# Kernel tuning notes

Hardware: AMD Instinct MI355X
Metric: run time of the kernel (lower is better)

The kernel has to match this reference:

```python
import jax, jax.numpy as jnp
import numpy as np
from functools import partial

M_HEADS, N_LEVELS, N_POINTS = 4, 3, 4


def conv2d(x, w, b, padding=1, dilation=1):
    y = jax.lax.conv_general_dilated(
        x, w, window_strides=(1, 1),
        padding=[(padding, padding), (padding, padding)],
        rhs_dilation=(dilation, dilation),
        dimension_numbers=('NCHW', 'OIHW', 'NCHW'))
    return y + b[None, :, None, None]


def lrelu(x):
    return jnp.where(x >= 0, x, 0.1 * x)


def _bilinear(img, gx, gy, zero_pad):
    # img: (C,H,W); gx,gy: arbitrary shape of pixel coordinates
    C, H, W = img.shape
    x0 = jnp.floor(gx); y0 = jnp.floor(gy)
    wx = gx - x0; wy = gy - y0
    def g(xi, yi):
        xc = jnp.clip(xi, 0, W - 1).astype(jnp.int32)
        yc = jnp.clip(yi, 0, H - 1).astype(jnp.int32)
        v = img[:, yc, xc]  # (C, ...)
        if zero_pad:
            ok = ((xi >= 0) & (xi <= W - 1) & (yi >= 0) & (yi <= H - 1)).astype(img.dtype)
            v = v * ok
        return v
    return (g(x0, y0) * ((1 - wx) * (1 - wy)) + g(x0 + 1, y0) * (wx * (1 - wy))
            + g(x0, y0 + 1) * ((1 - wx) * wy) + g(x0 + 1, y0 + 1) * (wx * wy))


def warp(x, flo):
    # torch grid_sample(padding_mode='border', align_corners=True) at coords grid+flow
    B, C, H, W = x.shape
    yy, xx = jnp.meshgrid(jnp.arange(H, dtype=x.dtype), jnp.arange(W, dtype=x.dtype), indexing='ij')
    gx = xx[None] + flo[:, 0]
    gy = yy[None] + flo[:, 1]
    return jax.vmap(partial(_bilinear, zero_pad=False))(x, gx, gy)


def _forward(frame, srcframe, flow_forward, flow_backward,
             emb_qk_w, emb_qk_b, emb_v_w, emb_v_b, so_w, so_b, aw_w, aw_b,
             vp_w, vp_b, op_w, op_b, ff_w, ff_b, ffn1_w, ffn1_b, ffn2_w, ffn2_b,
             fus_w, fus_b):
    M, L, P = M_HEADS, N_LEVELS, N_POINTS
    b, t, c, h, w = frame.shape
    HW = h * w
    D = c // M
    # flow-warped neighbor frames -> query embedding
    warp01 = warp(frame[:, 0], flow_backward[:, 0])
    warp21 = warp(frame[:, 2], flow_forward[:, 1])
    q_in = jnp.concatenate([warp01, frame[:, 1], warp21, flow_forward[:, 1], flow_backward[:, 0]], axis=1)
    query = lrelu(conv2d(q_in, emb_qk_w, emb_qk_b))  # (b, 3c, h, w)
    value = lrelu(conv2d(frame.reshape(b, t * c, h, w), emb_v_w, emb_v_b)).reshape(b, t, c, h, w)
    # MSDeformAttn_Fusion
    v = conv2d(value.reshape(b * t, c, h, w), vp_w, vp_b).reshape(b, t, c, h, w)  # value_proj per frame
    off = conv2d(query, so_w, so_b)   # (b, M*L*P*2, h, w)
    aw = conv2d(query, aw_w, aw_b)    # (b, M*L*P,   h, w)
    off = off.reshape(b, M * L * P * 2, HW).transpose(0, 2, 1).reshape(b, HW, M, L, P, 2)
    attn = aw.reshape(b, M * L * P, HW).transpose(0, 2, 1).reshape(b, HW, M, L * P)
    attn = jax.nn.softmax(attn, axis=-1).reshape(b, HW, M, L, P)
    # flow-guided offsets: [flow_backward10, 0, flow_forward12] per level
    flow_stack = jnp.stack([flow_backward[:, 0], jnp.zeros_like(flow_forward[:, 1]), flow_forward[:, 1]], axis=2)  # (b,2,L,h,w)
    off = off + flow_stack.reshape(b, 2, L, HW).transpose(0, 3, 2, 1)[:, :, None, :, None, :]
    # normalized reference points (valid ratios are all ones)
    ys, xs = jnp.meshgrid(jnp.arange(h, dtype=frame.dtype) + 0.5,
                          jnp.arange(w, dtype=frame.dtype) + 0.5, indexing='ij')
    ref = jnp.stack([xs.reshape(-1) / w, ys.reshape(-1) / h], axis=-1)  # (HW, 2)
    norm = jnp.array([w, h], dtype=frame.dtype)
    loc = ref[None, :, None, None, None, :] + off / norm  # (b,HW,M,L,P,2) in [0,1]
    # deformable gather: grid_sample(mode=bilinear, padding=zeros, align_corners=False)
    imgs = v.reshape(b, L, M, D, h, w).transpose(0, 2, 1, 3, 4, 5).reshape(b * M * L, D, h, w)
    locs = loc.transpose(0, 2, 3, 1, 4, 5).reshape(b * M * L, HW, P, 2)
    gx = locs[..., 0] * w - 0.5   # align_corners=False pixel coords
    gy = locs[..., 1] * h - 0.5
    sampled = jax.vmap(partial(_bilinear, zero_pad=True))(imgs, gx, gy)  # (b*M*L, D, HW, P)
    sampled = sampled.reshape(b, M, L, D, HW, P)
    out = jnp.einsum('nmldqp,nqmlp->nqmd', sampled, attn).reshape(b, HW, c)
    out = out.reshape(b, h, w, c).transpose(0, 3, 1, 2)
    out = conv2d(out, op_w, op_b)  # output_proj
    # post-attention feed-forward + fusion
    out = conv2d(out, ff_w, ff_b) + frame[:, 1]
    ffn = lrelu(conv2d(jnp.concatenate([out, srcframe[:, 1]], axis=1), ffn1_w, ffn1_b, padding=2, dilation=2))
    out = out + conv2d(ffn, ffn2_w, ffn2_b)
    out = lrelu(conv2d(out, fus_w, fus_b, padding=0))
    return out


def setup_inputs() -> dict:
    key = jax.random.key(0)
    ks = jax.random.split(key, 28)
    b, t, c, h, w = 2, 3, 32, 256, 256
    M, L, P = M_HEADS, N_LEVELS, N_POINTS
    def rn(k, shape, s=1.0):
        return jax.random.normal(k, shape, dtype=jnp.float32) * s
    return {
        'frame': rn(ks[0], (b, t, c, h, w)),
        'srcframe': rn(ks[1], (b, t, c, h, w)),
        'flow_forward': rn(ks[2], (b, 2, 2, h, w), 2.0),
        'flow_backward': rn(ks[3], (b, 2, 2, h, w), 2.0),
        'emb_qk_w': rn(ks[4], (3 * c, 3 * c + 4, 3, 3), 0.05), 'emb_qk_b': rn(ks[5], (3 * c,), 0.02),
        'emb_v_w': rn(ks[6], (3 * c, 3 * c, 3, 3), 0.05), 'emb_v_b': rn(ks[7], (3 * c,), 0.02),
        'so_w': rn(ks[8], (M * L * P * 2, 3 * c, 3, 3), 0.01), 'so_b': rn(ks[9], (M * L * P * 2,), 0.5),
        'aw_w': rn(ks[10], (M * L * P, 3 * c, 3, 3), 0.05), 'aw_b': rn(ks[11], (M * L * P,), 0.02),
        'vp_w': rn(ks[12], (c, c, 3, 3), 0.05), 'vp_b': rn(ks[13], (c,), 0.02),
        'op_w': rn(ks[14], (c, c, 3, 3), 0.05), 'op_b': rn(ks[15], (c,), 0.02),
        'ff_w': rn(ks[16], (c, c, 3, 3), 0.05), 'ff_b': rn(ks[17], (c,), 0.02),
        'ffn1_w': rn(ks[18], (c, 2 * c, 3, 3), 0.05), 'ffn1_b': rn(ks[19], (c,), 0.02),
        'ffn2_w': rn(ks[20], (c, c, 3, 3), 0.05), 'ffn2_b': rn(ks[21], (c,), 0.02),
        'fus_w': rn(ks[22], (c, c, 1, 1), 0.05), 'fus_b': rn(ks[23], (c,), 0.02),
    }


def reference(frame, srcframe, flow_forward, flow_backward,
              emb_qk_w, emb_qk_b, emb_v_w, emb_v_b, so_w, so_b, aw_w, aw_b,
              vp_w, vp_b, op_w, op_b, ff_w, ff_b, ffn1_w, ffn1_b, ffn2_w, ffn2_b,
              fus_w, fus_b):
    return _forward(frame, srcframe, flow_forward, flow_backward,
                    emb_qk_w, emb_qk_b, emb_v_w, emb_v_b, so_w, so_b, aw_w, aw_b,
                    vp_w, vp_b, op_w, op_b, ff_w, ff_b, ffn1_w, ffn1_b, ffn2_w, ffn2_b,
                    fus_w, fus_b)
```

## Files before the change

### kernel.cpp

```cpp
#include <hip/hip_runtime.h>
#include <cmath>

typedef _Float16 half_t;
typedef _Float16 half8 __attribute__((ext_vector_type(8)));
typedef _Float16 half4 __attribute__((ext_vector_type(4)));
typedef float floatx4 __attribute__((ext_vector_type(4)));

__device__ __forceinline__ float lrelu_f(float v) { return v >= 0.f ? v : 0.1f * v; }

template <int CIN, int COTOT>
__device__ __forceinline__ void pack_one(const float* __restrict__ w,
                                         half_t* __restrict__ o,
                                         int co_off, int co_n, int i)
{
    constexpr int NCB = (CIN + 31) / 32;
    int ci = i & 31;
    int t = i >> 5;
    int col = t % co_n; t /= co_n;
    int cb = t % NCB;
    int tap = t / NCB;
    int cg = cb * 32 + ci;
    float v = (cg < CIN) ? w[((long)col * CIN + cg) * 9 + tap] : 0.f;
    o[(((long)tap * NCB + cb) * COTOT + co_off + col) * 32 + ci] = (half_t)v;
}

__global__ __launch_bounds__(256) void prep_w_all(
    const float* __restrict__ qk, const float* __restrict__ ev,
    const float* __restrict__ so, const float* __restrict__ aw,
    const float* __restrict__ vp, const float* __restrict__ op,
    const float* __restrict__ ffw, const float* __restrict__ f1,
    const float* __restrict__ f2,
    half_t* wq, half_t* wv, half_t* wsoaw, half_t* wvp2, half_t* wop2,
    half_t* wff2, half_t* wffn1, half_t* wffn2)
{
    int i = blockIdx.x * 256 + threadIdx.x;
    constexpr int C0 = 110592;
    constexpr int C1 = C0 + 82944;
    constexpr int C2 = C1 + 82944;
    constexpr int C3 = C2 + 41472;
    constexpr int C4 = C3 + 9216;
    constexpr int C5 = C4 + 9216;
    constexpr int C6 = C5 + 9216;
    constexpr int C7 = C6 + 18432;
    constexpr int C8 = C7 + 9216;
    if (i < C0)      pack_one<100, 96>(qk, wq, 0, 96, i);
    else if (i < C1) pack_one<96, 96>(ev, wv, 0, 96, i - C0);
    else if (i < C2) pack_one<96, 144>(so, wsoaw, 0, 96, i - C1);
    else if (i < C3) pack_one<96, 144>(aw, wsoaw, 96, 48, i - C2);
    else if (i < C4) pack_one<32, 32>(vp, wvp2, 0, 32, i - C3);
    else if (i < C5) pack_one<32, 32>(op, wop2, 0, 32, i - C4);
    else if (i < C6) pack_one<32, 32>(ffw, wff2, 0, 32, i - C5);
    else if (i < C7) pack_one<64, 32>(f1, wffn1, 0, 32, i - C6);
    else if (i < C8) pack_one<32, 32>(f2, wffn2, 0, 32, i - C7);
}

__global__ __launch_bounds__(256) void copy_cl_kernel(
    const float* __restrict__ frame, const float* __restrict__ srcframe,
    const float* __restrict__ ff, const float* __restrict__ fb,
    half_t* __restrict__ qin, half_t* __restrict__ fcl,
    half_t* __restrict__ o3rec, int H, int W)
{
    const int HW = H * W;
    const int p = threadIdx.x >> 2, sub = threadIdx.x & 3;
    const int q = blockIdx.x * 64 + p;
    const int b = blockIdx.y;
    const long fbase = (long)b * 96 * HW;
    const long rq = ((long)b * HW + q) * 112;
    const long rf = ((long)b * HW + q) * 96;
    const long r3 = ((long)b * HW + q) * 64;

    half8 c0, c2;
    #pragma unroll
    for (int d = 0; d < 8; ++d) {
        c0[d] = (half_t)frame[fbase + (long)(sub * 8 + d) * HW + q];
        c2[d] = (half_t)frame[fbase + (long)(64 + sub * 8 + d) * HW + q];
    }
    *(half8*)&fcl[rf + sub * 8] = c0;
    *(half8*)&fcl[rf + 64 + sub * 8] = c2;

    half8 fv, sv;
    #pragma unroll
    for (int d = 0; d < 8; ++d) {
        long off = fbase + (long)(32 + sub * 8 + d) * HW + q;
        fv[d] = (half_t)frame[off];
        sv[d] = (half_t)srcframe[off];
    }
    *(half8*)&qin[rq + 32 + sub * 8] = fv;
    *(half8*)&fcl[rf + 32 + sub * 8] = fv;
    *(half8*)&o3rec[r3 + 32 + sub * 8] = sv;

    if (sub == 0) {
        half8 fl = {};
        fl[0] = (half_t)ff[((long)(b * 2 + 1) * 2 + 0) * HW + q];
        fl[1] = (half_t)ff[((long)(b * 2 + 1) * 2 + 1) * HW + q];
        fl[2] = (half_t)fb[((long)(b * 2 + 0) * 2 + 0) * HW + q];
        fl[3] = (half_t)fb[((long)(b * 2 + 0) * 2 + 1) * HW + q];
        *(half8*)&qin[rq + 96] = fl;
    } else if (sub == 1) {
        half8 z = {};
        *(half8*)&qin[rq + 104] = z;
    }
}

__global__ __launch_bounds__(256) void warp_cl_kernel(
    const half_t* __restrict__ fcl, const float* __restrict__ ff,
    const float* __restrict__ fb, half_t* __restrict__ qin, int H, int W)
{
    const int HW = H * W;
    const int p = threadIdx.x >> 2, sub = threadIdx.x & 3;
    const int q = blockIdx.x * 64 + p;
    const int b = blockIdx.y;
    const int x = q % W, y = q / W;
    const long rq = ((long)b * HW + q) * 112;
    const half_t* fc = fcl + (long)b * HW * 96;

    const float fb0x = fb[((long)(b * 2 + 0) * 2 + 0) * HW + q];
    const float fb0y = fb[((long)(b * 2 + 0) * 2 + 1) * HW + q];
    const float ff1x = ff[((long)(b * 2 + 1) * 2 + 0) * HW + q];
    const float ff1y = ff[((long)(b * 2 + 1) * 2 + 1) * HW + q];

    #pragma unroll
    for (int t = 0; t < 2; ++t) {
        const float fx = t ? ff1x : fb0x;
        const float fy = t ? ff1y : fb0y;
        const int coff = t ? 64 : 0;
        float gx = (float)x + fx, gy = (float)y + fy;
        float x0f = floorf(gx), y0f = floorf(gy);
        float wx = gx - x0f, wy = gy - y0f;
        int x0 = min(max((int)x0f, 0), W - 1);
        int x1 = min(max((int)x0f + 1, 0), W - 1);
        int y0 = min(max((int)y0f, 0), H - 1);
        int y1 = min(max((int)y0f + 1, 0), H - 1);
        float w00 = (1.f - wx) * (1.f - wy), w10 = wx * (1.f - wy);
        float w01 = (1.f - wx) * wy, w11 = wx * wy;

        half8 v00 = *(const half8*)&fc[(long)(y0 * W + x0) * 96 + coff + sub * 8];
        half8 v10 = *(const half8*)&fc[(long)(y0 * W + x1) * 96 + coff + sub * 8];
        half8 v01 = *(const half8*)&fc[(long)(y1 * W + x0) * 96 + coff + sub * 8];
        half8 v11 = *(const half8*)&fc[(long)(y1 * W + x1) * 96 + coff + sub * 8];

        half8 st;
        #pragma unroll
        for (int d = 0; d < 8; ++d) {
            float v = (float)v00[d] * w00 + (float)v10[d] * w10 +
                      (float)v01[d] * w01 + (float)v11[d] * w11;
            st[d] = (half_t)v;
        }
        *(half8*)&qin[rq + coff + sub * 8] = st;
    }
}

template <int CREC, int CIN, int COUT, int DIL, bool LRELU, int RESID_MODE,
          int OUTC, int SPLIT, bool OUT_TGROUP, int RESREC>
__global__ __launch_bounds__(512, 2) void conv3x3_cl(
    const half_t* __restrict__ in, long in_stride,
    const half_t* __restrict__ w16,
    const float* __restrict__ bias0, const float* __restrict__ bias1,
    const void* __restrict__ resid, long resid_stride,
    half_t* __restrict__ out, long out_stride, int H, int W)
{
    constexpr int NCB = (CIN + 31) / 32;
    constexpr int SX = 16 + 2 * DIL;
    constexpr int SY = 32 + 2 * DIL;
    constexpr int NF = COUT / 16;
    constexpr int COPAD = COUT + 2;
    constexpr int NLD = SY * SX * 4;
    constexpr int NITEM = (NLD + 511) / 512;
    constexpr int WCH = 9 * 4 * COPAD;
    constexpr int NWIT = (WCH + 511) / 512;
    __shared__ half_t sa[NLD * 8];
    __shared__ half_t sw[WCH * 8];

    const int n = blockIdx.y;
    const int tile = blockIdx.x;
    const int tx = tile & 15, ty = tile >> 4;
    const int tid = threadIdx.x;
    const int wv = tid >> 6, lane = tid & 63;
    const int cl = lane & 15, jk = lane >> 4;

    floatx4 acc[4][NF] = {};

    const int gy0 = ty * 32 - DIL, gx0 = tx * 16 - DIL;
    const int HWl = H * W;
    const half_t* ib = in + (long)n * in_stride;

    half8 ra[NITEM], rw[NWIT];
    auto LOADA = [&](int cb) {
        #pragma unroll
        for (int k = 0; k < NITEM; ++k) {
            int i = tid + k * 512;
            int pix = i >> 2;
            int sy = pix / SX, sx = pix - sy * SX;
            int gy = gy0 + sy, gx = gx0 + sx;
            int c_g = cb * 4 + (i & 3);
            half8 v = {};
            if (i < NLD && gy >= 0 && gy < H && gx >= 0 && gx < W &&
                (c_g * 8 + 8 <= CREC))
                v = *(const half8*)&ib[(long)(gy * W + gx) * CREC + c_g * 8];
            ra[k] = v;
        }
    };
    auto WRITEA = [&]() {
        #pragma unroll
        for (int k = 0; k < NITEM; ++k) {
            int i = tid + k * 512;
            if (i < NLD) {
                int pix = i >> 2, chunk = i & 3;
                *(half8*)&sa[((pix << 2) + (chunk ^ ((pix >> 1) & 3))) << 3] = ra[k];
            }
        }
    };
    auto LOADW = [&](int cb) {
        #pragma unroll
        for (int k = 0; k < NWIT; ++k) {
            int j = tid + k * 512;
            int tj = j / COPAD;
            int co = j - tj * COPAD;
            half8 v = {};
            if (j < WCH && co < COUT) {
                int tap = tj >> 2, jj = tj & 3;
                v = *(const half8*)&w16[(((long)tap * NCB + cb) * COUT + co) * 32 + jj * 8];
            }
            rw[k] = v;
        }
    };
    auto WRITEW = [&]() {
        #pragma unroll
        for (int k = 0; k < NWIT; ++k) {
            int j = tid + k * 512;
            if (j < WCH) *(half8*)&sw[j * 8] = rw[k];
        }
    };

    LOADA(0); LOADW(0);
    WRITEA(); WRITEW();
    __syncthreads();

    for (int cb = 0; cb < NCB; ++cb) {
        if (cb + 1 < NCB) { LOADA(cb + 1); LOADW(cb + 1); }

        #pragma unroll
        for (int tap = 0; tap < 9; ++tap) {
            const int ky = tap / 3, kx = tap % 3;
            half8 af[4];
            #pragma unroll
            for (int m = 0; m < 4; ++m) {
                int pix = (wv * 4 + m + ky * DIL) * SX + kx * DIL + cl;
                af[m] = *(const half8*)&sa[((pix << 2) + (jk ^ ((pix >> 1) & 3))) << 3];
            }
            const int wbase = ((tap << 2) | jk) * COPAD + cl;
            #pragma unroll
            for (int nn = 0; nn < NF; ++nn) {
                half8 bf = *(const half8*)&sw[(wbase + nn * 16) * 8];
                #pragma unroll
                for (int m = 0; m < 4; ++m)
                    acc[m][nn] = __builtin_amdgcn_mfma_f32_16x16x32_f16(
                        af[m], bf, acc[m][nn], 0, 0, 0);
            }
        }

        if (cb + 1 < NCB) {
            __syncthreads();
            WRITEA(); WRITEW();
            __syncthreads();
        }
    }

    const int x0 = tx * 16 + jk * 4;
    #pragma unroll
    for (int m = 0; m < 4; ++m) {
        const int yy = ty * 32 + wv * 4 + m;
        #pragma unroll
        for (int nn = 0; nn < NF; ++nn) {
            const int co = nn * 16 + cl;
            float bv = (co < SPLIT) ? bias0[co] : bias1[co - SPLIT];
            float r[4];
            #pragma unroll
            for (int i = 0; i < 4; ++i) r[i] = acc[m][nn][i] + bv;
            if constexpr (RESID_MODE == 1) {
                const float* rp = (const float*)resid + (long)n * resid_stride +
                                  (long)co * HWl + (long)yy * W + x0;
                float4 rv = *(const float4*)rp;
                r[0] += rv.x; r[1] += rv.y; r[2] += rv.z; r[3] += rv.w;
            } else if constexpr (RESID_MODE == 3) {
                const half_t* rp = (const half_t*)resid +
                                   ((long)n * HWl + (long)yy * W + x0) * RESREC + co;
                #pragma unroll
                for (int i = 0; i < 4; ++i) r[i] += (float)rp[i * RESREC];
            }
            if (LRELU) {
                #pragma unroll
                for (int i = 0; i < 4; ++i) r[i] = lrelu_f(r[i]);
            }
            if constexpr (OUT_TGROUP) {
                long base = ((long)(n * 3 + (co >> 5)) * HWl + (long)yy * W + x0) * 32 + (co & 31);
                #pragma unroll
                for (int i = 0; i < 4; ++i) out[base + i * 32] = (half_t)r[i];
            } else {
                long base = (long)n * out_stride + ((long)yy * W + x0) * OUTC + co;
                #pragma unroll
                for (int i = 0; i < 4; ++i) out[base + i * OUTC] = (half_t)r[i];
            }
        }
    }
}

__global__ __launch_bounds__(256) void deform_v3(
    const half_t* __restrict__ v_cl, const half_t* __restrict__ offaw,
    const float* __restrict__ ff, const float* __restrict__ fb,
    half_t* __restrict__ out1, int H, int W)
{
    const int HW = H * W;
    const int bid = blockIdx.x;
    const int swz = (bid & 7) * 128 + (bid >> 3);
    const int tx = swz & 31, ty = swz >> 5;
    const int b = blockIdx.y;
    const int p = threadIdx.x >> 2;
    const int m = threadIdx.x & 3;
    const int x = tx * 8 + (p & 7), y = ty * 8 + (p >> 3);
    const int q = y * W + x;

    const half_t* rec = &offaw[((long)b * HW + q) * 144];
    half8 offv[3];
    #pragma unroll
    for (int i = 0; i < 3; ++i) offv[i] = *(const half8*)&rec[m * 24 + i * 8];
    half4 awv[3];
    #pragma unroll
    for (int i = 0; i < 3; ++i) awv[i] = *(const half4*)&rec[96 + m * 12 + i * 4];

    float fbx = fb[((long)(b * 2 + 0) * 2 + 0) * HW + q];
    float fby = fb[((long)(b * 2 + 0) * 2 + 1) * HW + q];
    float ffx = ff[((long)(b * 2 + 1) * 2 + 0) * HW + q];
    float ffy = ff[((long)(b * 2 + 1) * 2 + 1) * HW + q];

    float a[12], mx = -1e30f;
    #pragma unroll
    for (int i = 0; i < 12; ++i) {
        a[i] = (float)awv[i >> 2][i & 3];
        mx = fmaxf(mx, a[i]);
    }
    float s = 0.f;
    #pragma unroll
    for (int i = 0; i < 12; ++i) { a[i] = expf(a[i] - mx); s += a[i]; }
    float inv = 1.f / s;

    float o[8] = {0, 0, 0, 0, 0, 0, 0, 0};
    #pragma unroll
    for (int l = 0; l < 3; ++l) {
        float fx = (l == 0) ? fbx : (l == 2) ? ffx : 0.f;
        float fy = (l == 0) ? fby : (l == 2) ? ffy : 0.f;
        const half_t* img = v_cl + (long)(b * 3 + l) * HW * 32 + m * 8;
        #pragma unroll
        for (int pp = 0; pp < 4; ++pp) {
            int oc = (l * 4 + pp) * 2;
            float gx = (float)x + (float)offv[oc >> 3][oc & 7] + fx;
            float gy = (float)y + (float)offv[(oc + 1) >> 3][(oc + 1) & 7] + fy;
            float wgt = a[l * 4 + pp] * inv;
            float x0f = floorf(gx), y0f = floorf(gy);
            float wx = gx - x0f, wy = gy - y0f;
            int x0 = (int)x0f, y0 = (int)y0f;
            #pragma unroll
            for (int t_ = 0; t_ < 4; ++t_) {
                int xi = x0 + (t_ & 1), yi = y0 + (t_ >> 1);
                float wt = ((t_ & 1) ? wx : 1.f - wx) *
                           ((t_ >> 1) ? wy : 1.f - wy) * wgt;
                if (xi >= 0 && xi < W && yi >= 0 && yi < H) {
                    const half8 vv = *(const half8*)&img[(long)(yi * W + xi) * 32];
                    #pragma unroll
                    for (int d = 0; d < 8; ++d) o[d] = fmaf(wt, (float)vv[d], o[d]);
                }
            }
        }
    }
    half8 st;
    #pragma unroll
    for (int d = 0; d < 8; ++d) st[d] = (half_t)o[d];
    *(half8*)&out1[((long)b * HW + q) * 32 + m * 8] = st;
}

__global__ __launch_bounds__(256) void conv1x1_f16(
    const half_t* __restrict__ in, const float* __restrict__ w,
    const float* __restrict__ bias, float* __restrict__ out, int HW)
{
    int q = blockIdx.x * 256 + threadIdx.x;
    if (q >= HW) return;
    long b = blockIdx.y;
    const half8* ip = (const half8*)&in[((long)b * HW + q) * 32];
    half8 vv[4];
    #pragma unroll
    for (int i = 0; i < 4; ++i) vv[i] = ip[i];
    float v[32];
    #pragma unroll
    for (int ci = 0; ci < 32; ++ci) v[ci] = (float)vv[ci >> 3][ci & 7];
    float* ob = out + b * 32 * HW;
    #pragma unroll
    for (int co = 0; co < 32; ++co) {
        float acc = bias[co];
        #pragma unroll
        for (int ci = 0; ci < 32; ++ci) acc = fmaf(w[co * 32 + ci], v[ci], acc);
        ob[(long)co * HW + q] = lrelu_f(acc);
    }
}

extern "C" void kernel_launch(void* const* d_in, const int* in_sizes, int n_in,
                              void* d_out, int out_size, void* d_ws, size_t ws_size,
                              hipStream_t stream)
{
    (void)in_sizes; (void)n_in; (void)out_size; (void)ws_size;
    const int H = 256, W = 256, HW = H * W, B = 2;

    const float* frame    = (const float*)d_in[0];
    const float* srcframe = (const float*)d_in[1];
    const float* ff       = (const float*)d_in[2];
    const float* fb       = (const float*)d_in[3];
    const float* emb_qk_w = (const float*)d_in[4];
    const float* emb_qk_b = (const float*)d_in[5];
    const float* emb_v_w  = (const float*)d_in[6];
    const float* emb_v_b  = (const float*)d_in[7];
    const float* so_w     = (const float*)d_in[8];
    const float* so_b     = (const float*)d_in[9];
    const float* aw_w     = (const float*)d_in[10];
    const float* aw_b     = (const float*)d_in[11];
    const float* vp_w     = (const float*)d_in[12];
    const float* vp_b     = (const float*)d_in[13];
    const float* op_w     = (const float*)d_in[14];
    const float* op_b     = (const float*)d_in[15];
    const float* ff_w     = (const float*)d_in[16];
    const float* ff_b     = (const float*)d_in[17];
    const float* ffn1_w   = (const float*)d_in[18];
    const float* ffn1_b   = (const float*)d_in[19];
    const float* ffn2_w   = (const float*)d_in[20];
    const float* ffn2_b   = (const float*)d_in[21];
    const float* fus_w    = (const float*)d_in[22];
    const float* fus_b    = (const float*)d_in[23];

    half_t* hw = (half_t*)d_ws;
    half_t* q_in_cl = hw;
    half_t* fcl     = hw + 14680064L;
    half_t* value_g = hw + 27262976L;
    half_t* offaw   = hw + 14680064L;
    half_t* query_c = hw + 39845888L;
    half_t* v_cl    = hw + 52428800L;
    half_t* out1    = hw + 65011712L;
    half_t* out2    = hw + 69206016L;
    half_t* o3rec   = hw + 73400320L;
    half_t* ffnb    = hw + 81788928L;
    half_t* out4    = hw + 85983232L;
    half_t* wq      = hw + 90177536L;
    half_t* wv      = hw + 90288128L;
    half_t* wsoaw   = hw + 90371072L;
    half_t* wvp     = hw + 90495488L;
    half_t* wop     = hw + 90504704L;
    half_t* wff     = hw + 90513920L;
    half_t* wffn1   = hw + 90523136L;
    half_t* wffn2   = hw + 90541568L;

    dim3 blk(256);
    dim3 cblk(512);
    dim3 convGrid(128, B);

    prep_w_all<<<(373248 + 255) / 256, blk, 0, stream>>>(
        emb_qk_w, emb_v_w, so_w, aw_w, vp_w, op_w, ff_w, ffn1_w, ffn2_w,
        wq, wv, wsoaw, wvp, wop, wff, wffn1, wffn2);

    copy_cl_kernel<<<dim3(HW / 64, B), blk, 0, stream>>>(frame, srcframe, ff, fb,
                                                         q_in_cl, fcl, o3rec, H, W);
    warp_cl_kernel<<<dim3(HW / 64, B), blk, 0, stream>>>(fcl, ff, fb, q_in_cl, H, W);

    conv3x3_cl<112, 100, 96, 1, true, 0, 96, 96, false, 0>
        <<<convGrid, cblk, 0, stream>>>(q_in_cl, (long)HW * 112, wq, emb_qk_b, nullptr,
                                        nullptr, 0, query_c, (long)HW * 96, H, W);
    conv3x3_cl<96, 96, 96, 1, true, 0, 32, 96, true, 0>
        <<<convGrid, cblk, 0, stream>>>(fcl, (long)HW * 96, wv, emb_v_b, nullptr,
                                        nullptr, 0, value_g, 0, H, W);
    conv3x3_cl<32, 32, 32, 1, false, 0, 32, 32, false, 0>
        <<<dim3(128, 6), cblk, 0, stream>>>(value_g, (long)HW * 32, wvp, vp_b, nullptr,
                                            nullptr, 0, v_cl, (long)HW * 32, H, W);
    conv3x3_cl<96, 96, 144, 1, false, 0, 144, 96, false, 0>
        <<<convGrid, cblk, 0, stream>>>(query_c, (long)HW * 96, wsoaw, so_b, aw_b,
                                        nullptr, 0, offaw, (long)HW * 144, H, W);
    deform_v3<<<dim3(1024, B), blk, 0, stream>>>(v_cl, offaw, ff, fb, out1, H, W);
    conv3x3_cl<32, 32, 32, 1, false, 0, 32, 32, false, 0>
        <<<convGrid, cblk, 0, stream>>>(out1, (long)HW * 32, wop, op_b, nullptr,
                                        nullptr, 0, out2, (long)HW * 32, H, W);
    conv3x3_cl<32, 32, 32, 1, false, 1, 64, 32, false, 0>
        <<<convGrid, cblk, 0, stream>>>(out2, (long)HW * 32, wff, ff_b, nullptr,
                                        frame + 32L * HW, 96L * HW, o3rec, (long)HW * 64, H, W);
    conv3x3_cl<64, 64, 32, 2, true, 0, 32, 32, false, 0>
        <<<convGrid, cblk, 0, stream>>>(o3rec, (long)HW * 64, wffn1, ffn1_b, nullptr,
                                        nullptr, 0, ffnb, (long)HW * 32, H, W);
    conv3x3_cl<32, 32, 32, 1, false, 3, 32, 32, false, 64>
        <<<convGrid, cblk, 0, stream>>>(ffnb, (long)HW * 32, wffn2, ffn2_b, nullptr,
                                        o3rec, 0, out4, (long)HW * 32, H, W);
    conv1x1_f16<<<dim3(HW / 256, B), blk, 0, stream>>>(out4, fus_w, fus_b,
                                                       (float*)d_out, HW);
}
```

Before: 318.8 us.

## Shrink conv tiles to 16x16 and split output channels across wave pairs

The 3x3 convolution kernel now uses 16x16 pixel tiles, so the grid doubles to 256 blocks per image. Its eight waves are split into four row groups and two output-channel halves, so each wave holds half the accumulators. Register-staged double buffering is replaced by direct global-to-LDS staging between barriers. The aim is more blocks for occupancy and fewer registers per wave, at the cost of more halo reloads, duplicated weight staging per block, and no overlap of loads with MFMA work.

```diff
diff --git a/kernel.cpp b/kernel.cpp
--- a/kernel.cpp
+++ b/kernel.cpp
@@ -160,14 +160,12 @@
     half_t* __restrict__ out, long out_stride, int H, int W)
 {
     constexpr int NCB = (CIN + 31) / 32;
-    constexpr int SX = 16 + 2 * DIL;
-    constexpr int SY = 32 + 2 * DIL;
+    constexpr int S = 16 + 2 * DIL;
     constexpr int NF = COUT / 16;
+    constexpr int NFH = (NF + 1) / 2;
     constexpr int COPAD = COUT + 2;
-    constexpr int NLD = SY * SX * 4;
-    constexpr int NITEM = (NLD + 511) / 512;
+    constexpr int NLD = S * S * 4;
     constexpr int WCH = 9 * 4 * COPAD;
-    constexpr int NWIT = (WCH + 511) / 512;
     __shared__ half_t sa[NLD * 8];
     __shared__ half_t sw[WCH * 8];
 
@@ -176,92 +174,68 @@
     const int tx = tile & 15, ty = tile >> 4;
     const int tid = threadIdx.x;
     const int wv = tid >> 6, lane = tid & 63;
+    const int rowgrp = wv >> 1, cogrp = wv & 1;
     const int cl = lane & 15, jk = lane >> 4;
-
-    floatx4 acc[4][NF] = {};
-
-    const int gy0 = ty * 32 - DIL, gx0 = tx * 16 - DIL;
+    const int nf0 = cogrp * NFH;
+
+    floatx4 acc[4][NFH] = {};
+
+    const int gy0 = ty * 16 - DIL, gx0 = tx * 16 - DIL;
     const int HWl = H * W;
     const half_t* ib = in + (long)n * in_stride;
 
-    half8 ra[NITEM], rw[NWIT];
-    auto LOADA = [&](int cb) {
-        #pragma unroll
-        for (int k = 0; k < NITEM; ++k) {
-            int i = tid + k * 512;
-            int pix = i >> 2;
-            int sy = pix / SX, sx = pix - sy * SX;
+    auto STAGE = [&](int cb) {
+        for (int i = tid; i < NLD; i += 512) {
+            int pix = i >> 2, chunk = i & 3;
+            int sy = pix / S, sx = pix - sy * S;
             int gy = gy0 + sy, gx = gx0 + sx;
-            int c_g = cb * 4 + (i & 3);
+            int c_g = cb * 4 + chunk;
             half8 v = {};
-            if (i < NLD && gy >= 0 && gy < H && gx >= 0 && gx < W &&
-                (c_g * 8 + 8 <= CREC))
+            if (gy >= 0 && gy < H && gx >= 0 && gx < W && (c_g * 8 + 8 <= CREC))
                 v = *(const half8*)&ib[(long)(gy * W + gx) * CREC + c_g * 8];
-            ra[k] = v;
-        }
-    };
-    auto WRITEA = [&]() {
-        #pragma unroll
-        for (int k = 0; k < NITEM; ++k) {
-            int i = tid + k * 512;
-            if (i < NLD) {
-                int pix = i >> 2, chunk = i & 3;
-                *(half8*)&sa[((pix << 2) + (chunk ^ ((pix >> 1) & 3))) << 3] = ra[k];
-            }
-        }
-    };
-    auto LOADW = [&](int cb) {
-        #pragma unroll
-        for (int k = 0; k < NWIT; ++k) {
-            int j = tid + k * 512;
+            *(half8*)&sa[((pix << 2) + (chunk ^ ((pix >> 1) & 3))) << 3] = v;
+        }
+        for (int j = tid; j < WCH; j += 512) {
             int tj = j / COPAD;
             int co = j - tj * COPAD;
             half8 v = {};
-            if (j < WCH && co < COUT) {
+            if (co < COUT) {
                 int tap = tj >> 2, jj = tj & 3;
                 v = *(const half8*)&w16[(((long)tap * NCB + cb) * COUT + co) * 32 + jj * 8];
             }
-            rw[k] = v;
+            *(half8*)&sw[j * 8] = v;
         }
     };
-    auto WRITEW = [&]() {
-        #pragma unroll
-        for (int k = 0; k < NWIT; ++k) {
-            int j = tid + k * 512;
-            if (j < WCH) *(half8*)&sw[j * 8] = rw[k];
-        }
-    };
-
-    LOADA(0); LOADW(0);
-    WRITEA(); WRITEW();
+
+    STAGE(0);
     __syncthreads();
 
     for (int cb = 0; cb < NCB; ++cb) {
-        if (cb + 1 < NCB) { LOADA(cb + 1); LOADW(cb + 1); }
-
         #pragma unroll
         for (int tap = 0; tap < 9; ++tap) {
             const int ky = tap / 3, kx = tap % 3;
             half8 af[4];
             #pragma unroll
             for (int m = 0; m < 4; ++m) {
-                int pix = (wv * 4 + m + ky * DIL) * SX + kx * DIL + cl;
+                int pix = (rowgrp * 4 + m + ky * DIL) * S + kx * DIL + cl;
                 af[m] = *(const half8*)&sa[((pix << 2) + (jk ^ ((pix >> 1) & 3))) << 3];
             }
             const int wbase = ((tap << 2) | jk) * COPAD + cl;
             #pragma unroll
-            for (int nn = 0; nn < NF; ++nn) {
-                half8 bf = *(const half8*)&sw[(wbase + nn * 16) * 8];
-                #pragma unroll
-                for (int m = 0; m < 4; ++m)
-                    acc[m][nn] = __builtin_amdgcn_mfma_f32_16x16x32_f16(
-                        af[m], bf, acc[m][nn], 0, 0, 0);
+            for (int f = 0; f < NFH; ++f) {
+                if (nf0 + f < NF) {
+                    half8 bf = *(const half8*)&sw[(wbase + (nf0 + f) * 16) * 8];
+                    #pragma unroll
+                    for (int m = 0; m < 4; ++m)
+                        acc[m][f] = __builtin_amdgcn_mfma_f32_16x16x32_f16(
+                            af[m], bf, acc[m][f], 0, 0, 0);
+                }
             }
         }
 
         if (cb + 1 < NCB) {
             __syncthreads();
-            WRITEA(); WRITEW();
+            STAGE(cb + 1);
             __syncthreads();
         }
     }
@@ -269,14 +243,15 @@
     const int x0 = tx * 16 + jk * 4;
     #pragma unroll
     for (int m = 0; m < 4; ++m) {
-        const int yy = ty * 32 + wv * 4 + m;
+        const int yy = ty * 16 + rowgrp * 4 + m;
         #pragma unroll
-        for (int nn = 0; nn < NF; ++nn) {
-            const int co = nn * 16 + cl;
+        for (int f = 0; f < NFH; ++f) {
+            if (nf0 + f >= NF) continue;
+            const int co = (nf0 + f) * 16 + cl;
             float bv = (co < SPLIT) ? bias0[co] : bias1[co - SPLIT];
             float r[4];
             #pragma unroll
-            for (int i = 0; i < 4; ++i) r[i] = acc[m][nn][i] + bv;
+            for (int i = 0; i < 4; ++i) r[i] = acc[m][f][i] + bv;
             if constexpr (RESID_MODE == 1) {
                 const float* rp = (const float*)resid + (long)n * resid_stride +
                                   (long)co * HWl + (long)yy * W + x0;
@@ -457,7 +432,7 @@
 
     dim3 blk(256);
     dim3 cblk(512);
-    dim3 convGrid(128, B);
+    dim3 convGrid(256, B);
 
     prep_w_all<<<(373248 + 255) / 256, blk, 0, stream>>>(
         emb_qk_w, emb_v_w, so_w, aw_w, vp_w, op_w, ff_w, ffn1_w, ffn2_w,
@@ -474,7 +449,7 @@
         <<<convGrid, cblk, 0, stream>>>(fcl, (long)HW * 96, wv, emb_v_b, nullptr,
                                         nullptr, 0, value_g, 0, H, W);
     conv3x3_cl<32, 32, 32, 1, false, 0, 32, 32, false, 0>
-        <<<dim3(128, 6), cblk, 0, stream>>>(value_g, (long)HW * 32, wvp, vp_b, nullptr,
+        <<<dim3(256, 6), cblk, 0, stream>>>(value_g, (long)HW * 32, wvp, vp_b, nullptr,
                                             nullptr, 0, v_cl, (long)HW * 32, H, W);
     conv3x3_cl<96, 96, 144, 1, false, 0, 144, 96, false, 0>
         <<<convGrid, cblk, 0, stream>>>(query_c, (long)HW * 96, wsoaw, so_b, aw_b,
```

Measured after the change: 303.4 us. -4.8%, faster.
